# Performance work log

Measured on AMD Instinct MI355X. Metric: run time of the kernel, lower is better.

The kernel has to match this reference:

```python
import jax, jax.numpy as jnp
import numpy as np

N_NODES = 50000
N_REL = 3
N_EDGES = 640000
D_IN = 128
D_HID = 128
D_OUT = 32
N_LAYERS = 2


def setup_inputs() -> dict:
    key = jax.random.key(0)
    ks = jax.random.split(key, 7)
    x = jax.random.normal(ks[0], (N_NODES, D_IN), dtype=jnp.float32)
    edge_index = jax.random.randint(ks[1], (N_REL, 2, N_EDGES), 0, N_NODES, dtype=jnp.int32)
    sc = 1.0 / np.sqrt(D_HID)
    W_neigh = jax.random.normal(ks[2], (N_LAYERS, N_REL, D_IN, D_HID), dtype=jnp.float32) * sc
    W_root = jax.random.normal(ks[3], (N_LAYERS, N_REL, D_IN, D_HID), dtype=jnp.float32) * sc
    b_conv = jax.random.normal(ks[4], (N_LAYERS, N_REL, D_HID), dtype=jnp.float32) * sc
    lin_W = jax.random.normal(ks[5], (D_HID, D_OUT), dtype=jnp.float32) * sc
    lin_b = jax.random.normal(ks[6], (D_OUT,), dtype=jnp.float32) * sc
    return {"x": x, "edge_index": edge_index, "W_neigh": W_neigh,
            "W_root": W_root, "b_conv": b_conv, "lin_W": lin_W, "lin_b": lin_b}


def _sage_hetero_layer(h, edge_index, Wn_l, Wr_l, b_l):
    # h: [N, d_in]; edge_index: [n_rel, 2, E]
    N = h.shape[0]
    acc = jnp.zeros((N, Wn_l.shape[-1]), dtype=h.dtype)
    for r in range(edge_index.shape[0]):  # small fixed relation set
        src, dst = edge_index[r, 0], edge_index[r, 1]
        msg = h[src]                                         # gather [E, d]
        summed = jax.ops.segment_sum(msg, dst, num_segments=N)
        deg = jax.ops.segment_sum(jnp.ones(src.shape, h.dtype), dst, num_segments=N)
        mean = summed / jnp.maximum(deg, 1.0)[:, None]       # SAGE mean aggr
        # SAGEConv: lin_l(aggr) + lin_r(x); bias lives in lin_l
        acc = acc + mean @ Wn_l[r] + h @ Wr_l[r] + b_l[r]    # HeteroConv sum across relations
    return acc


def reference(x, edge_index, W_neigh, W_root, b_conv, lin_W, lin_b):
    h = x
    for l in range(W_neigh.shape[0]):
        h = jax.nn.relu(_sage_hetero_layer(h, edge_index, W_neigh[l], W_root[l], b_conv[l]))
    return h @ lin_W + lin_b
```

## Files before the change

kernel.cpp:

```cpp
#include <hip/hip_runtime.h>

#define NN 50000
#define NE 640000
#define NR 3
#define DH 128
#define ET (NR * NE)

#define BK 256
#define NBK 196
#define NBT (NR * NBK)
#define NCH 512
#define CH (ET / NCH)
#define CAPB 4096

typedef __attribute__((ext_vector_type(8))) short short8;
typedef __attribute__((ext_vector_type(4))) float f32x4;
typedef __attribute__((ext_vector_type(2))) float f32x2;

__device__ __forceinline__ float bf2f(uint u) { return __uint_as_float(u << 16); }
__device__ __forceinline__ uint f2bf(float f) {
    uint u = __float_as_uint(f);
    u += 0x7fff + ((u >> 16) & 1);
    return u >> 16;
}
__device__ __forceinline__ uint pack2(float a, float b) { return f2bf(a) | (f2bf(b) << 16); }
__device__ __forceinline__ f32x2 pkadd(f32x2 a, f32x2 b) {
    f32x2 d;
    asm("v_pk_add_f32 %0, %1, %2" : "=v"(d) : "v"(a), "v"(b));
    return d;
}
__device__ __forceinline__ f32x2 f8lo(uint u) {
    return __builtin_amdgcn_cvt_pk_f32_fp8(u, false);
}
__device__ __forceinline__ f32x2 f8hi(uint u) {
    return __builtin_amdgcn_cvt_pk_f32_fp8(u, true);
}
__device__ __forceinline__ uint pack4f8(float a, float b, float c, float d) {
    int w = __builtin_amdgcn_cvt_pk_fp8_f32(a, b, 0, false);
    w = __builtin_amdgcn_cvt_pk_fp8_f32(c, d, w, true);
    return (uint)w;
}

__global__ __launch_bounds__(256) void prep_hist(const float* __restrict__ x,
                                                 const int* __restrict__ ei,
                                                 const float* __restrict__ Wn,
                                                 const float* __restrict__ Wr,
                                                 const float* __restrict__ bc,
                                                 const float* __restrict__ linW,
                                                 unsigned char* __restrict__ xf8,
                                                 ushort* __restrict__ Wpack,
                                                 float* __restrict__ bsum,
                                                 int* __restrict__ gcnt) {
    int bid = blockIdx.x;
    int t = threadIdx.x;
    if (bid < NCH) {
        __shared__ int hist[NBT];
        for (int i = t; i < NBT; i += 256) hist[i] = 0;
        __syncthreads();
        int e0 = bid * CH;
        for (int i = t; i < CH; i += 256) {
            int e = e0 + i;
            int r = (e >= 2 * NE) ? 2 : (e >= NE ? 1 : 0);
            int le = e - r * NE;
            int dst = ei[r * 2 * NE + NE + le];
            atomicAdd(&hist[r * NBK + (dst >> 8)], 1);
        }
        __syncthreads();
        for (int i = t; i < NBT; i += 256) gcnt[bid * NBT + i] = hist[i];
    } else if (bid < NCH + 6251) {
        int gid = (bid - NCH) * 256 + t;
        if (gid >= NN * DH / 4) return;
        float4 v = ((const float4*)x)[gid];
        ((uint*)xf8)[gid] = pack4f8(v.x, v.y, v.z, v.w);
    } else if (bid < NCH + 6251 + 66) {
        int tid = (bid - NCH - 6251) * 256 + t;
        if (tid >= 264 * 64) return;
        int f = tid >> 6, lane = tid & 63;
        int l15 = lane & 15, l4 = lane >> 4;
        ushort hi8[8], lo8[8];
        if (f < 256) {
            int layer = f >> 7, seg = (f >> 5) & 3, kc = (f >> 3) & 3, nb = f & 7;
            int col = nb * 16 + l15;
            int kb = kc * 32 + l4 * 8;
#pragma unroll
            for (int e = 0; e < 8; ++e) {
                int k = kb + e;
                float v;
                if (seg < 3) {
                    v = Wn[(((size_t)layer * 3 + seg) * 128 + k) * 128 + col];
                } else {
                    const float* base = Wr + (size_t)layer * 3 * 16384;
                    v = base[k * 128 + col] + base[16384 + k * 128 + col] +
                        base[32768 + k * 128 + col];
                }
                uint h = f2bf(v);
                float rem = v - bf2f(h);
                hi8[e] = (ushort)h;
                lo8[e] = (ushort)f2bf(rem);
            }
        } else {
            int g = f - 256;
            int kc = g >> 1, nb = g & 1;
            int col = nb * 16 + l15;
            int kb = kc * 32 + l4 * 8;
#pragma unroll
            for (int e = 0; e < 8; ++e) {
                float v = linW[(kb + e) * 32 + col];
                uint h = f2bf(v);
                float rem = v - bf2f(h);
                hi8[e] = (ushort)h;
                lo8[e] = (ushort)f2bf(rem);
            }
        }
        *(short8*)(Wpack + (size_t)f * 1024 + lane * 8) = *(short8*)hi8;
        *(short8*)(Wpack + (size_t)f * 1024 + 512 + lane * 8) = *(short8*)lo8;
    } else {
        int l = t >> 7, j = t & 127;
        const float* bb = bc + l * 3 * DH;
        bsum[t] = bb[j] + bb[DH + j] + bb[2 * DH + j];
    }
}

__global__ __launch_bounds__(256) void cscan_kernel(const int* __restrict__ gcnt,
                                                    int* __restrict__ gbase,
                                                    int* __restrict__ btot) {
    int b = blockIdx.x, t = threadIdx.x;
    int v0 = gcnt[(2 * t) * NBT + b];
    int v1 = gcnt[(2 * t + 1) * NBT + b];
    int s = v0 + v1;
    int lane = t & 63, w = t >> 6;
    int sc = s;
#pragma unroll
    for (int d = 1; d < 64; d <<= 1) {
        int u = __shfl_up(sc, d);
        if (lane >= d) sc += u;
    }
    __shared__ int ws[4];
    if (lane == 63) ws[w] = sc;
    __syncthreads();
    int add = 0;
#pragma unroll
    for (int q = 0; q < 3; ++q)
        if (q < w) add += ws[q];
    int incl = sc + add;
    int excl = incl - s;
    gbase[(2 * t) * NBT + b] = excl;
    gbase[(2 * t + 1) * NBT + b] = excl + v0;
    if (t == 255) btot[b] = incl;
}

__global__ __launch_bounds__(256) void scatter_kernel(const int* __restrict__ ei,
                                                      const int* __restrict__ gbase,
                                                      uint* __restrict__ pairs) {
    __shared__ int cur[NBT];
    int g = blockIdx.x, t = threadIdx.x;
    for (int i = t; i < NBT; i += 256) cur[i] = i * CAPB + gbase[g * NBT + i];
    __syncthreads();
    int e0 = g * CH;
    for (int i = t; i < CH; i += 256) {
        int e = e0 + i;
        int r = (e >= 2 * NE) ? 2 : (e >= NE ? 1 : 0);
        int le = e - r * NE;
        int src = ei[r * 2 * NE + le];
        int dst = ei[r * 2 * NE + NE + le];
        int b = r * NBK + (dst >> 8);
        int pos = atomicAdd(&cur[b], 1);
        pairs[pos] = ((uint)src << 8) | (uint)(dst & 255u);
    }
}

__global__ __launch_bounds__(256) void csr_kernel(const uint* __restrict__ pairs,
                                                  const int* __restrict__ btot,
                                                  int* __restrict__ csr,
                                                  int2* __restrict__ od) {
    int b = blockIdx.x;
    int r = b / NBK;
    int n0 = (b - r * NBK) * BK;
    int cnt = btot[b];
    int base = b * CAPB;
    int t = threadIdx.x;

    __shared__ int hist[BK];
    __shared__ int cur[BK];
    __shared__ int ws[4];
    hist[t] = 0;
    __syncthreads();
    const uint* pp = pairs + base;
    for (int i = t; i < cnt; i += 256) atomicAdd(&hist[pp[i] & 255u], 1);
    __syncthreads();

    int lane = t & 63, w = t >> 6;
    int v = hist[t], s = v;
#pragma unroll
    for (int d = 1; d < 64; d <<= 1) {
        int u = __shfl_up(s, d);
        if (lane >= d) s += u;
    }
    if (lane == 63) ws[w] = s;
    __syncthreads();
    int add = 0;
#pragma unroll
    for (int q = 0; q < 3; ++q)
        if (q < w) add += ws[q];
    int excl = s + add - v;

    int node = n0 + t;
    if (node < NN) od[r * NN + node] = make_int2(base + excl, v);
    cur[t] = excl;
    __syncthreads();

    for (int i = t; i < cnt; i += 256) {
        uint pk = pp[i];
        int pos = atomicAdd(&cur[pk & 255u], 1);
        csr[base + pos] = (int)(pk >> 8);
    }
}

__global__ __launch_bounds__(256) void aggr_kernel(const unsigned char* __restrict__ tb8,
                                                   ushort* __restrict__ mean_b,
                                                   const int* __restrict__ csr,
                                                   const int2* __restrict__ od) {
    int gtask = (blockIdx.x * 256 + threadIdx.x) >> 3;
    if (gtask >= NR * NN) return;
    int cs = threadIdx.x & 7;
    int2 v2 = od[gtask];
    int base = v2.x, d = v2.y;
    const int* lst = csr + base;
    const unsigned char* tbc = tb8 + cs * 16;

    f32x2 a2[8] = {{0.f, 0.f}, {0.f, 0.f}, {0.f, 0.f}, {0.f, 0.f},
                   {0.f, 0.f}, {0.f, 0.f}, {0.f, 0.f}, {0.f, 0.f}};
    for (int e = 0; e < d; e += 8) {
        uint4 q[8];
#pragma unroll
        for (int k = 0; k < 8; ++k) {
            int ee = e + k;
            int idx = lst[min(ee, d - 1)];
            uint4 v = *(const uint4*)(tbc + (size_t)idx * DH);
            bool ok = ee < d;
            q[k].x = ok ? v.x : 0u;
            q[k].y = ok ? v.y : 0u;
            q[k].z = ok ? v.z : 0u;
            q[k].w = ok ? v.w : 0u;
        }
#pragma unroll
        for (int k = 0; k < 8; ++k) {
            a2[0] = pkadd(a2[0], f8lo(q[k].x));
            a2[1] = pkadd(a2[1], f8hi(q[k].x));
            a2[2] = pkadd(a2[2], f8lo(q[k].y));
            a2[3] = pkadd(a2[3], f8hi(q[k].y));
            a2[4] = pkadd(a2[4], f8lo(q[k].z));
            a2[5] = pkadd(a2[5], f8hi(q[k].z));
            a2[6] = pkadd(a2[6], f8lo(q[k].w));
            a2[7] = pkadd(a2[7], f8hi(q[k].w));
        }
    }
    float inv = 1.f / fmaxf((float)d, 1.f);
    uint4 o0, o1;
    o0.x = pack2(a2[0].x * inv, a2[0].y * inv);
    o0.y = pack2(a2[1].x * inv, a2[1].y * inv);
    o0.z = pack2(a2[2].x * inv, a2[2].y * inv);
    o0.w = pack2(a2[3].x * inv, a2[3].y * inv);
    o1.x = pack2(a2[4].x * inv, a2[4].y * inv);
    o1.y = pack2(a2[5].x * inv, a2[5].y * inv);
    o1.z = pack2(a2[6].x * inv, a2[6].y * inv);
    o1.w = pack2(a2[7].x * inv, a2[7].y * inv);
    ushort* mp = mean_b + (size_t)gtask * DH + cs * 16;
    *(uint4*)mp = o0;
    *(uint4*)(mp + 8) = o1;
}

template <bool LAST>
__global__ __launch_bounds__(256) void gemm_mfma(
    const float* __restrict__ xroot,
    const ushort* __restrict__ tbroot,
    const ushort* __restrict__ mean_b,
    void* __restrict__ h_out,
    unsigned char* __restrict__ h1f8,
    const ushort* __restrict__ Wp,
    const float* __restrict__ bsum,
    const ushort* __restrict__ lWp,
    const float* __restrict__ linb)
{
    __shared__ ushort As[64][136];

    const int t = threadIdx.x, lane = t & 63, w = t >> 6;
    const int l15 = lane & 15, l4 = lane >> 4;
    const int row0 = blockIdx.x * 64;

    f32x4 acc[4][2];
    {
        float4 b0 = *(const float4*)(bsum + (2 * w) * 16 + l4 * 4);
        float4 b1 = *(const float4*)(bsum + (2 * w + 1) * 16 + l4 * 4);
#pragma unroll
        for (int rt = 0; rt < 4; ++rt) {
            acc[rt][0] = f32x4{b0.x, b0.y, b0.z, b0.w};
            acc[rt][1] = f32x4{b1.x, b1.y, b1.z, b1.w};
        }
    }

    for (int seg = 0; seg < 4; ++seg) {
        __syncthreads();
#pragma unroll
        for (int i = 0; i < 4; ++i) {
            int q = i * 256 + t;
            int r = q >> 4, c = q & 15;
            int node = row0 + r;
            uint4 v = make_uint4(0, 0, 0, 0);
            if (node < NN) {
                if (seg < NR) {
                    v = *(const uint4*)(mean_b + ((size_t)seg * NN + node) * DH + c * 8);
                } else if constexpr (!LAST) {
                    float4 f0 = *(const float4*)(xroot + (size_t)node * DH + c * 8);
                    float4 f1 = *(const float4*)(xroot + (size_t)node * DH + c * 8 + 4);
                    v.x = pack2(f0.x, f0.y);
                    v.y = pack2(f0.z, f0.w);
                    v.z = pack2(f1.x, f1.y);
                    v.w = pack2(f1.z, f1.w);
                } else {
                    v = *(const uint4*)(tbroot + (size_t)node * DH + c * 8);
                }
            }
            *(uint4*)(&As[r][c * 8]) = v;
        }
        __syncthreads();
        const ushort* wseg = Wp + (size_t)seg * 32768;
#pragma unroll
        for (int kc = 0; kc < 4; ++kc) {
            const ushort* wkc = wseg + kc * 8192;
            short8 bh0 = *(const short8*)(wkc + (2 * w) * 1024 + lane * 8);
            short8 bl0 = *(const short8*)(wkc + (2 * w) * 1024 + 512 + lane * 8);
            short8 bh1 = *(const short8*)(wkc + (2 * w + 1) * 1024 + lane * 8);
            short8 bl1 = *(const short8*)(wkc + (2 * w + 1) * 1024 + 512 + lane * 8);
#pragma unroll
            for (int rt = 0; rt < 4; ++rt) {
                short8 a = *(const short8*)(&As[rt * 16 + l15][kc * 32 + l4 * 8]);
                acc[rt][0] = __builtin_amdgcn_mfma_f32_16x16x32_bf16(bh0, a, acc[rt][0], 0, 0, 0);
                acc[rt][0] = __builtin_amdgcn_mfma_f32_16x16x32_bf16(bl0, a, acc[rt][0], 0, 0, 0);
                acc[rt][1] = __builtin_amdgcn_mfma_f32_16x16x32_bf16(bh1, a, acc[rt][1], 0, 0, 0);
                acc[rt][1] = __builtin_amdgcn_mfma_f32_16x16x32_bf16(bl1, a, acc[rt][1], 0, 0, 0);
            }
        }
    }

    if constexpr (!LAST) {
        ushort* hb = (ushort*)h_out;
#pragma unroll
        for (int rt = 0; rt < 4; ++rt) {
            int node = row0 + rt * 16 + l15;
            if (node < NN) {
#pragma unroll
                for (int j = 0; j < 2; ++j) {
                    int c0 = (2 * w + j) * 16 + l4 * 4;
                    float r0 = fmaxf(acc[rt][j][0], 0.f);
                    float r1 = fmaxf(acc[rt][j][1], 0.f);
                    float r2 = fmaxf(acc[rt][j][2], 0.f);
                    float r3 = fmaxf(acc[rt][j][3], 0.f);
                    uint2 o;
                    o.x = pack2(r0, r1);
                    o.y = pack2(r2, r3);
                    *(uint2*)(hb + (size_t)node * DH + c0) = o;
                    *(uint*)(h1f8 + (size_t)node * DH + c0) = pack4f8(r0, r1, r2, r3);
                }
            }
        }
    } else {
        __syncthreads();
#pragma unroll
        for (int rt = 0; rt < 4; ++rt) {
            int rl = rt * 16 + l15;
#pragma unroll
            for (int j = 0; j < 2; ++j) {
                int c0 = (2 * w + j) * 16 + l4 * 4;
                uint2 o;
                o.x = pack2(fmaxf(acc[rt][j][0], 0.f), fmaxf(acc[rt][j][1], 0.f));
                o.y = pack2(fmaxf(acc[rt][j][2], 0.f), fmaxf(acc[rt][j][3], 0.f));
                *(uint2*)(&As[rl][c0]) = o;
            }
        }
        __syncthreads();
        f32x4 acc2[2];
        {
            float4 c0 = *(const float4*)(linb + l4 * 4);
            float4 c1 = *(const float4*)(linb + 16 + l4 * 4);
            acc2[0] = f32x4{c0.x, c0.y, c0.z, c0.w};
            acc2[1] = f32x4{c1.x, c1.y, c1.z, c1.w};
        }
#pragma unroll
        for (int kc = 0; kc < 4; ++kc) {
            short8 a = *(const short8*)(&As[w * 16 + l15][kc * 32 + l4 * 8]);
#pragma unroll
            for (int j = 0; j < 2; ++j) {
                short8 bh = *(const short8*)(lWp + (kc * 2 + j) * 1024 + lane * 8);
                short8 bl = *(const short8*)(lWp + (kc * 2 + j) * 1024 + 512 + lane * 8);
                acc2[j] = __builtin_amdgcn_mfma_f32_16x16x32_bf16(bh, a, acc2[j], 0, 0, 0);
                acc2[j] = __builtin_amdgcn_mfma_f32_16x16x32_bf16(bl, a, acc2[j], 0, 0, 0);
            }
        }
        float* outp = (float*)h_out;
        int node = row0 + w * 16 + l15;
        if (node < NN) {
#pragma unroll
            for (int j = 0; j < 2; ++j) {
                *(f32x4*)(outp + (size_t)node * 32 + j * 16 + l4 * 4) = acc2[j];
            }
        }
    }
}

extern "C" void kernel_launch(void* const* d_in, const int* in_sizes, int n_in,
                              void* d_out, int out_size, void* d_ws, size_t ws_size,
                              hipStream_t stream) {
    const float* x = (const float*)d_in[0];
    const int* ei = (const int*)d_in[1];
    const float* Wn = (const float*)d_in[2];
    const float* Wr = (const float*)d_in[3];
    const float* bc = (const float*)d_in[4];
    const float* linW = (const float*)d_in[5];
    const float* linb = (const float*)d_in[6];
    float* out = (float*)d_out;

    char* p = (char*)d_ws;
    int* gcnt = (int*)p;     p += (size_t)NCH * NBT * 4;
    int* gbase = (int*)p;    p += (size_t)NCH * NBT * 4;
    int* btot = (int*)p;     p += 4096;
    int2* od = (int2*)p;     p += (size_t)NR * NN * 8;
    int* csr = (int*)p;      p += (size_t)NBT * CAPB * 4;
    ushort* Wpack = (ushort*)p; p += (size_t)264 * 1024 * 2;
    float* bsum = (float*)p; p += 4096;
    unsigned char* f8tab = (unsigned char*)p; p += (size_t)NN * DH;
    ushort* h1b = (ushort*)p; p += (size_t)NN * DH * 2;
    ushort* mean_b = (ushort*)p; p += (size_t)NR * NN * DH * 2;
    uint* pairs = (uint*)mean_b;

    prep_hist<<<NCH + 6251 + 66 + 1, 256, 0, stream>>>(x, ei, Wn, Wr, bc, linW,
                                                       f8tab, Wpack, bsum, gcnt);
    cscan_kernel<<<NBT, 256, 0, stream>>>(gcnt, gbase, btot);
    scatter_kernel<<<NCH, 256, 0, stream>>>(ei, gbase, pairs);
    csr_kernel<<<NBT, 256, 0, stream>>>(pairs, btot, csr, od);

    int lb = (NN + 63) / 64;
    int ag = (NR * NN * 8 + 255) / 256;

    aggr_kernel<<<ag, 256, 0, stream>>>(f8tab, mean_b, csr, od);
    gemm_mfma<false><<<lb, 256, 0, stream>>>(x, nullptr, mean_b, h1b, f8tab,
                                             Wpack, bsum, nullptr, nullptr);
    aggr_kernel<<<ag, 256, 0, stream>>>(f8tab, mean_b, csr, od);
    gemm_mfma<true><<<lb, 256, 0, stream>>>(nullptr, h1b, mean_b, out, nullptr,
                                            Wpack + (size_t)128 * 1024, bsum + DH,
                                            Wpack + (size_t)256 * 1024, linb);
}
```

Measured before the change: 172.2 us.

## Fuse neighbor mean aggregation into the per-layer MFMA GEMM kernel

Drops the separate aggregation kernel and instead has each 512-thread block compute the per-relation fp8 gather-mean for its 64 nodes directly into shared memory, then feed it to the MFMA GEMM. This removes the write and re-read of the large bf16 mean buffer (3×N×128) and two kernel launches per forward pass. Each wave now covers 16 output columns instead of 32. The cost is that the irregular gather latency is serialized with the GEMM inside each block, with fewer blocks and less latency hiding than the standalone aggregation launch. The h1 fp8 table is now kept in a separate scratch area so the first layer's gather source is not overwritten while other blocks still read it.

After: 194.5 us. 13.0% more time.

```diff
diff --git a/kernel.cpp b/kernel.cpp
--- a/kernel.cpp
+++ b/kernel.cpp
@@ -216,67 +216,15 @@
     }
 }
 
-__global__ __launch_bounds__(256) void aggr_kernel(const unsigned char* __restrict__ tb8,
-                                                   ushort* __restrict__ mean_b,
-                                                   const int* __restrict__ csr,
-                                                   const int2* __restrict__ od) {
-    int gtask = (blockIdx.x * 256 + threadIdx.x) >> 3;
-    if (gtask >= NR * NN) return;
-    int cs = threadIdx.x & 7;
-    int2 v2 = od[gtask];
-    int base = v2.x, d = v2.y;
-    const int* lst = csr + base;
-    const unsigned char* tbc = tb8 + cs * 16;
-
-    f32x2 a2[8] = {{0.f, 0.f}, {0.f, 0.f}, {0.f, 0.f}, {0.f, 0.f},
-                   {0.f, 0.f}, {0.f, 0.f}, {0.f, 0.f}, {0.f, 0.f}};
-    for (int e = 0; e < d; e += 8) {
-        uint4 q[8];
-#pragma unroll
-        for (int k = 0; k < 8; ++k) {
-            int ee = e + k;
-            int idx = lst[min(ee, d - 1)];
-            uint4 v = *(const uint4*)(tbc + (size_t)idx * DH);
-            bool ok = ee < d;
-            q[k].x = ok ? v.x : 0u;
-            q[k].y = ok ? v.y : 0u;
-            q[k].z = ok ? v.z : 0u;
-            q[k].w = ok ? v.w : 0u;
-        }
-#pragma unroll
-        for (int k = 0; k < 8; ++k) {
-            a2[0] = pkadd(a2[0], f8lo(q[k].x));
-            a2[1] = pkadd(a2[1], f8hi(q[k].x));
-            a2[2] = pkadd(a2[2], f8lo(q[k].y));
-            a2[3] = pkadd(a2[3], f8hi(q[k].y));
-            a2[4] = pkadd(a2[4], f8lo(q[k].z));
-            a2[5] = pkadd(a2[5], f8hi(q[k].z));
-            a2[6] = pkadd(a2[6], f8lo(q[k].w));
-            a2[7] = pkadd(a2[7], f8hi(q[k].w));
-        }
-    }
-    float inv = 1.f / fmaxf((float)d, 1.f);
-    uint4 o0, o1;
-    o0.x = pack2(a2[0].x * inv, a2[0].y * inv);
-    o0.y = pack2(a2[1].x * inv, a2[1].y * inv);
-    o0.z = pack2(a2[2].x * inv, a2[2].y * inv);
-    o0.w = pack2(a2[3].x * inv, a2[3].y * inv);
-    o1.x = pack2(a2[4].x * inv, a2[4].y * inv);
-    o1.y = pack2(a2[5].x * inv, a2[5].y * inv);
-    o1.z = pack2(a2[6].x * inv, a2[6].y * inv);
-    o1.w = pack2(a2[7].x * inv, a2[7].y * inv);
-    ushort* mp = mean_b + (size_t)gtask * DH + cs * 16;
-    *(uint4*)mp = o0;
-    *(uint4*)(mp + 8) = o1;
-}
-
 template <bool LAST>
-__global__ __launch_bounds__(256) void gemm_mfma(
+__global__ __launch_bounds__(512) void layer_fused(
+    const unsigned char* __restrict__ tb8,
     const float* __restrict__ xroot,
     const ushort* __restrict__ tbroot,
-    const ushort* __restrict__ mean_b,
     void* __restrict__ h_out,
     unsigned char* __restrict__ h1f8,
+    const int* __restrict__ csr,
+    const int2* __restrict__ od,
     const ushort* __restrict__ Wp,
     const float* __restrict__ bsum,
     const ushort* __restrict__ lWp,
@@ -286,59 +234,99 @@
 
     const int t = threadIdx.x, lane = t & 63, w = t >> 6;
     const int l15 = lane & 15, l4 = lane >> 4;
+    const int g = t >> 3, cs = t & 7;
     const int row0 = blockIdx.x * 64;
 
-    f32x4 acc[4][2];
+    f32x4 acc[4];
     {
-        float4 b0 = *(const float4*)(bsum + (2 * w) * 16 + l4 * 4);
-        float4 b1 = *(const float4*)(bsum + (2 * w + 1) * 16 + l4 * 4);
-#pragma unroll
-        for (int rt = 0; rt < 4; ++rt) {
-            acc[rt][0] = f32x4{b0.x, b0.y, b0.z, b0.w};
-            acc[rt][1] = f32x4{b1.x, b1.y, b1.z, b1.w};
-        }
+        float4 bv = *(const float4*)(bsum + w * 16 + l4 * 4);
+#pragma unroll
+        for (int rt = 0; rt < 4; ++rt) acc[rt] = f32x4{bv.x, bv.y, bv.z, bv.w};
     }
 
     for (int seg = 0; seg < 4; ++seg) {
         __syncthreads();
-#pragma unroll
-        for (int i = 0; i < 4; ++i) {
-            int q = i * 256 + t;
-            int r = q >> 4, c = q & 15;
-            int node = row0 + r;
-            uint4 v = make_uint4(0, 0, 0, 0);
+        if (seg < NR) {
+            int node = row0 + g;
+            uint4 o0 = make_uint4(0, 0, 0, 0), o1 = make_uint4(0, 0, 0, 0);
             if (node < NN) {
-                if (seg < NR) {
-                    v = *(const uint4*)(mean_b + ((size_t)seg * NN + node) * DH + c * 8);
-                } else if constexpr (!LAST) {
-                    float4 f0 = *(const float4*)(xroot + (size_t)node * DH + c * 8);
-                    float4 f1 = *(const float4*)(xroot + (size_t)node * DH + c * 8 + 4);
-                    v.x = pack2(f0.x, f0.y);
-                    v.y = pack2(f0.z, f0.w);
-                    v.z = pack2(f1.x, f1.y);
-                    v.w = pack2(f1.z, f1.w);
-                } else {
-                    v = *(const uint4*)(tbroot + (size_t)node * DH + c * 8);
+                int2 v2 = od[seg * NN + node];
+                int base = v2.x, d = v2.y;
+                const int* lst = csr + base;
+                const unsigned char* tbc = tb8 + cs * 16;
+                f32x2 a2[8] = {{0.f, 0.f}, {0.f, 0.f}, {0.f, 0.f}, {0.f, 0.f},
+                               {0.f, 0.f}, {0.f, 0.f}, {0.f, 0.f}, {0.f, 0.f}};
+                for (int e = 0; e < d; e += 8) {
+                    uint4 q[8];
+#pragma unroll
+                    for (int k = 0; k < 8; ++k) {
+                        int ee = e + k;
+                        int idx = lst[min(ee, d - 1)];
+                        uint4 v = *(const uint4*)(tbc + (size_t)idx * DH);
+                        bool ok = ee < d;
+                        q[k].x = ok ? v.x : 0u;
+                        q[k].y = ok ? v.y : 0u;
+                        q[k].z = ok ? v.z : 0u;
+                        q[k].w = ok ? v.w : 0u;
+                    }
+#pragma unroll
+                    for (int k = 0; k < 8; ++k) {
+                        a2[0] = pkadd(a2[0], f8lo(q[k].x));
+                        a2[1] = pkadd(a2[1], f8hi(q[k].x));
+                        a2[2] = pkadd(a2[2], f8lo(q[k].y));
+                        a2[3] = pkadd(a2[3], f8hi(q[k].y));
+                        a2[4] = pkadd(a2[4], f8lo(q[k].z));
+                        a2[5] = pkadd(a2[5], f8hi(q[k].z));
+                        a2[6] = pkadd(a2[6], f8lo(q[k].w));
+                        a2[7] = pkadd(a2[7], f8hi(q[k].w));
+                    }
                 }
-            }
-            *(uint4*)(&As[r][c * 8]) = v;
+                float inv = 1.f / fmaxf((float)d, 1.f);
+                o0.x = pack2(a2[0].x * inv, a2[0].y * inv);
+                o0.y = pack2(a2[1].x * inv, a2[1].y * inv);
+                o0.z = pack2(a2[2].x * inv, a2[2].y * inv);
+                o0.w = pack2(a2[3].x * inv, a2[3].y * inv);
+                o1.x = pack2(a2[4].x * inv, a2[4].y * inv);
+                o1.y = pack2(a2[5].x * inv, a2[5].y * inv);
+                o1.z = pack2(a2[6].x * inv, a2[6].y * inv);
+                o1.w = pack2(a2[7].x * inv, a2[7].y * inv);
+            }
+            *(uint4*)(&As[g][cs * 16]) = o0;
+            *(uint4*)(&As[g][cs * 16 + 8]) = o1;
+        } else {
+#pragma unroll
+            for (int it = 0; it < 2; ++it) {
+                int q = it * 512 + t;
+                int r = q >> 4, c = q & 15;
+                int node = row0 + r;
+                uint4 v = make_uint4(0, 0, 0, 0);
+                if (node < NN) {
+                    if constexpr (!LAST) {
+                        float4 f0 = *(const float4*)(xroot + (size_t)node * DH + c * 8);
+                        float4 f1 = *(const float4*)(xroot + (size_t)node * DH + c * 8 + 4);
+                        v.x = pack2(f0.x, f0.y);
+                        v.y = pack2(f0.z, f0.w);
+                        v.z = pack2(f1.x, f1.y);
+                        v.w = pack2(f1.z, f1.w);
+                    } else {
+                        v = *(const uint4*)(tbroot + (size_t)node * DH + c * 8);
+                    }
+                }
+                *(uint4*)(&As[r][c * 8]) = v;
+            }
         }
         __syncthreads();
         const ushort* wseg = Wp + (size_t)seg * 32768;
 #pragma unroll
         for (int kc = 0; kc < 4; ++kc) {
-            const ushort* wkc = wseg + kc * 8192;
-            short8 bh0 = *(const short8*)(wkc + (2 * w) * 1024 + lane * 8);
-            short8 bl0 = *(const short8*)(wkc + (2 * w) * 1024 + 512 + lane * 8);
-            short8 bh1 = *(const short8*)(wkc + (2 * w + 1) * 1024 + lane * 8);
-            short8 bl1 = *(const short8*)(wkc + (2 * w + 1) * 1024 + 512 + lane * 8);
+            const ushort* wkc = wseg + kc * 8192 + w * 1024;
+            short8 bh = *(const short8*)(wkc + lane * 8);
+            short8 bl = *(const short8*)(wkc + 512 + lane * 8);
 #pragma unroll
             for (int rt = 0; rt < 4; ++rt) {
                 short8 a = *(const short8*)(&As[rt * 16 + l15][kc * 32 + l4 * 8]);
-                acc[rt][0] = __builtin_amdgcn_mfma_f32_16x16x32_bf16(bh0, a, acc[rt][0], 0, 0, 0);
-                acc[rt][0] = __builtin_amdgcn_mfma_f32_16x16x32_bf16(bl0, a, acc[rt][0], 0, 0, 0);
-                acc[rt][1] = __builtin_amdgcn_mfma_f32_16x16x32_bf16(bh1, a, acc[rt][1], 0, 0, 0);
-                acc[rt][1] = __builtin_amdgcn_mfma_f32_16x16x32_bf16(bl1, a, acc[rt][1], 0, 0, 0);
+                acc[rt] = __builtin_amdgcn_mfma_f32_16x16x32_bf16(bh, a, acc[rt], 0, 0, 0);
+                acc[rt] = __builtin_amdgcn_mfma_f32_16x16x32_bf16(bl, a, acc[rt], 0, 0, 0);
             }
         }
     }
@@ -349,61 +337,47 @@
         for (int rt = 0; rt < 4; ++rt) {
             int node = row0 + rt * 16 + l15;
             if (node < NN) {
-#pragma unroll
-                for (int j = 0; j < 2; ++j) {
-                    int c0 = (2 * w + j) * 16 + l4 * 4;
-                    float r0 = fmaxf(acc[rt][j][0], 0.f);
-                    float r1 = fmaxf(acc[rt][j][1], 0.f);
-                    float r2 = fmaxf(acc[rt][j][2], 0.f);
-                    float r3 = fmaxf(acc[rt][j][3], 0.f);
-                    uint2 o;
-                    o.x = pack2(r0, r1);
-                    o.y = pack2(r2, r3);
-                    *(uint2*)(hb + (size_t)node * DH + c0) = o;
-                    *(uint*)(h1f8 + (size_t)node * DH + c0) = pack4f8(r0, r1, r2, r3);
-                }
+                int c0 = w * 16 + l4 * 4;
+                float r0 = fmaxf(acc[rt][0], 0.f);
+                float r1 = fmaxf(acc[rt][1], 0.f);
+                float r2 = fmaxf(acc[rt][2], 0.f);
+                float r3 = fmaxf(acc[rt][3], 0.f);
+                uint2 o;
+                o.x = pack2(r0, r1);
+                o.y = pack2(r2, r3);
+                *(uint2*)(hb + (size_t)node * DH + c0) = o;
+                *(uint*)(h1f8 + (size_t)node * DH + c0) = pack4f8(r0, r1, r2, r3);
             }
         }
     } else {
         __syncthreads();
 #pragma unroll
         for (int rt = 0; rt < 4; ++rt) {
-            int rl = rt * 16 + l15;
-#pragma unroll
-            for (int j = 0; j < 2; ++j) {
-                int c0 = (2 * w + j) * 16 + l4 * 4;
-                uint2 o;
-                o.x = pack2(fmaxf(acc[rt][j][0], 0.f), fmaxf(acc[rt][j][1], 0.f));
-                o.y = pack2(fmaxf(acc[rt][j][2], 0.f), fmaxf(acc[rt][j][3], 0.f));
-                *(uint2*)(&As[rl][c0]) = o;
-            }
-        }
-        __syncthreads();
-        f32x4 acc2[2];
+            uint2 o;
+            o.x = pack2(fmaxf(acc[rt][0], 0.f), fmaxf(acc[rt][1], 0.f));
+            o.y = pack2(fmaxf(acc[rt][2], 0.f), fmaxf(acc[rt][3], 0.f));
+            *(uint2*)(&As[rt * 16 + l15][w * 16 + l4 * 4]) = o;
+        }
+        __syncthreads();
+        int rt2 = w >> 1, nb = w & 1;
+        f32x4 acc2;
         {
-            float4 c0 = *(const float4*)(linb + l4 * 4);
-            float4 c1 = *(const float4*)(linb + 16 + l4 * 4);
-            acc2[0] = f32x4{c0.x, c0.y, c0.z, c0.w};
-            acc2[1] = f32x4{c1.x, c1.y, c1.z, c1.w};
+            float4 c0 = *(const float4*)(linb + nb * 16 + l4 * 4);
+            acc2 = f32x4{c0.x, c0.y, c0.z, c0.w};
         }
 #pragma unroll
         for (int kc = 0; kc < 4; ++kc) {
-            short8 a = *(const short8*)(&As[w * 16 + l15][kc * 32 + l4 * 8]);
-#pragma unroll
-            for (int j = 0; j < 2; ++j) {
-                short8 bh = *(const short8*)(lWp + (kc * 2 + j) * 1024 + lane * 8);
-                short8 bl = *(const short8*)(lWp + (kc * 2 + j) * 1024 + 512 + lane * 8);
-                acc2[j] = __builtin_amdgcn_mfma_f32_16x16x32_bf16(bh, a, acc2[j], 0, 0, 0);
-                acc2[j] = __builtin_amdgcn_mfma_f32_16x16x32_bf16(bl, a, acc2[j], 0, 0, 0);
-            }
+            short8 a = *(const short8*)(&As[rt2 * 16 + l15][kc * 32 + l4 * 8]);
+            const ushort* lw = lWp + (kc * 2 + nb) * 1024;
+            short8 bh = *(const short8*)(lw + lane * 8);
+            short8 bl = *(const short8*)(lw + 512 + lane * 8);
+            acc2 = __builtin_amdgcn_mfma_f32_16x16x32_bf16(bh, a, acc2, 0, 0, 0);
+            acc2 = __builtin_amdgcn_mfma_f32_16x16x32_bf16(bl, a, acc2, 0, 0, 0);
         }
         float* outp = (float*)h_out;
-        int node = row0 + w * 16 + l15;
+        int node = row0 + rt2 * 16 + l15;
         if (node < NN) {
-#pragma unroll
-            for (int j = 0; j < 2; ++j) {
-                *(f32x4*)(outp + (size_t)node * 32 + j * 16 + l4 * 4) = acc2[j];
-            }
+            *(f32x4*)(outp + (size_t)node * 32 + nb * 16 + l4 * 4) = acc2;
         }
     }
 }
@@ -428,25 +402,23 @@
     int* csr = (int*)p;      p += (size_t)NBT * CAPB * 4;
     ushort* Wpack = (ushort*)p; p += (size_t)264 * 1024 * 2;
     float* bsum = (float*)p; p += 4096;
-    unsigned char* f8tab = (unsigned char*)p; p += (size_t)NN * DH;
+    unsigned char* xf8 = (unsigned char*)p; p += (size_t)NN * DH;
     ushort* h1b = (ushort*)p; p += (size_t)NN * DH * 2;
-    ushort* mean_b = (ushort*)p; p += (size_t)NR * NN * DH * 2;
-    uint* pairs = (uint*)mean_b;
+    char* scratch = p;       p += (size_t)ET * 4;
+    uint* pairs = (uint*)scratch;
+    unsigned char* h1f8 = (unsigned char*)scratch;
 
     prep_hist<<<NCH + 6251 + 66 + 1, 256, 0, stream>>>(x, ei, Wn, Wr, bc, linW,
-                                                       f8tab, Wpack, bsum, gcnt);
+                                                       xf8, Wpack, bsum, gcnt);
     cscan_kernel<<<NBT, 256, 0, stream>>>(gcnt, gbase, btot);
     scatter_kernel<<<NCH, 256, 0, stream>>>(ei, gbase, pairs);
     csr_kernel<<<NBT, 256, 0, stream>>>(pairs, btot, csr, od);
 
     int lb = (NN + 63) / 64;
-    int ag = (NR * NN * 8 + 255) / 256;
-
-    aggr_kernel<<<ag, 256, 0, stream>>>(f8tab, mean_b, csr, od);
-    gemm_mfma<false><<<lb, 256, 0, stream>>>(x, nullptr, mean_b, h1b, f8tab,
-                                             Wpack, bsum, nullptr, nullptr);
-    aggr_kernel<<<ag, 256, 0, stream>>>(f8tab, mean_b, csr, od);
-    gemm_mfma<true><<<lb, 256, 0, stream>>>(nullptr, h1b, mean_b, out, nullptr,
-                                            Wpack + (size_t)128 * 1024, bsum + DH,
-                                            Wpack + (size_t)256 * 1024, linb);
-}
+
+    layer_fused<false><<<lb, 512, 0, stream>>>(xf8, x, nullptr, h1b, h1f8, csr, od,
+                                               Wpack, bsum, nullptr, nullptr);
+    layer_fused<true><<<lb, 512, 0, stream>>>(h1f8, nullptr, h1b, out, nullptr, csr, od,
+                                              Wpack + (size_t)128 * 1024, bsum + DH,
+                                              Wpack + (size_t)256 * 1024, linb);
+}
```
